# Kernel optimization log

Measured on AMD Instinct MI355X. Metric: run time of the kernel, lower is better.

Reference implementation:

```python
import jax, jax.numpy as jnp
import numpy as np

N_NODES = 51200      # 128 graphs * 400 ROIs
N_ROI = 400
HID = 64             # 'batch_size' arg of the torch module = hidden channels = n_timepoints
N_EDGES = 1638400    # avg degree 32
N_CLASSES = 2
NEG_SLOPE = 0.01


def setup_inputs():
    key = jax.random.key(0)
    ks = jax.random.split(key, 20)
    s = 0.05
    inp = {
        'x': jax.random.normal(ks[0], (N_NODES, HID), dtype=jnp.float32),
        'edge_index': jax.random.randint(ks[1], (2, N_EDGES), 0, N_NODES, dtype=jnp.int64),
        'edge_weight': jax.random.uniform(ks[2], (N_EDGES,), dtype=jnp.float32),
        # GCNConv weights stored [in, out]; biases [out]
        'W1': jax.random.normal(ks[3], (HID, HID), dtype=jnp.float32) * s,
        'b1': jnp.zeros((HID,), jnp.float32),
        'W2': jax.random.normal(ks[4], (HID, HID), dtype=jnp.float32) * s,
        'b2': jnp.zeros((HID,), jnp.float32),
        'W3': jax.random.normal(ks[5], (HID, HID), dtype=jnp.float32) * s,
        'b3': jnp.zeros((HID,), jnp.float32),
        'W4': jax.random.normal(ks[6], (HID, HID), dtype=jnp.float32) * s,
        'b4': jnp.zeros((HID,), jnp.float32),
        'fc1_w': jax.random.normal(ks[7], (N_ROI * HID, 256), dtype=jnp.float32) * 0.01,
        'fc1_b': jnp.zeros((256,), jnp.float32),
        'fc2_w': jax.random.normal(ks[8], (256, 128), dtype=jnp.float32) * s,
        'fc2_b': jnp.zeros((128,), jnp.float32),
        'fc3_w': jax.random.normal(ks[9], (128, N_CLASSES), dtype=jnp.float32) * s,
        'fc3_b': jnp.zeros((N_CLASSES,), jnp.float32),
    }
    return inp


def _gcn_norm(edge_index, edge_weight, n):
    # PyG GCNConv: add self-loops (weight 1), symmetric D^-1/2 A D^-1/2 normalization
    loop = jnp.arange(n, dtype=edge_index.dtype)
    src = jnp.concatenate([edge_index[0], loop])
    dst = jnp.concatenate([edge_index[1], loop])
    w = jnp.concatenate([edge_weight, jnp.ones((n,), edge_weight.dtype)])
    deg = jax.ops.segment_sum(w, dst, num_segments=n)
    dis = jnp.where(deg > 0, jax.lax.rsqrt(jnp.maximum(deg, 1e-30)), 0.0)
    norm = dis[src] * w * dis[dst]
    return src, dst, norm


def _conv(h, W, b, src, dst, norm, n):
    h = h @ W                                   # [N, out]
    msg = h[src] * norm[:, None]                # gather + scale
    out = jax.ops.segment_sum(msg, dst, num_segments=n) + b
    return out


def _leaky(v):
    return jnp.where(v >= 0, v, NEG_SLOPE * v)


def _head(h, fc1_w, fc1_b, fc2_w, fc2_b, fc3_w, fc3_b):
    # global_mean_pool with batch = arange(N) is identity; pool == reshape to graphs
    g = h.reshape(-1, N_ROI * HID)              # [G, n_roi*hid]
    g = g @ fc1_w + fc1_b                       # dropout is eval-mode identity
    g = g @ fc2_w + fc2_b
    g = g @ fc3_w + fc3_b
    return g


def reference(x, edge_index, edge_weight, W1, b1, W2, b2, W3, b3, W4, b4,
              fc1_w, fc1_b, fc2_w, fc2_b, fc3_w, fc3_b):
    n = x.shape[0]
    src, dst, norm = _gcn_norm(edge_index, edge_weight, n)
    h = _leaky(_conv(x, W1, b1, src, dst, norm, n))
    h = _leaky(_conv(h, W2, b2, src, dst, norm, n))
    h = _leaky(_conv(h, W3, b3, src, dst, norm, n))
    h = _leaky(_conv(h, W4, b4, src, dst, norm, n))
    logits = _head(h, fc1_w, fc1_b, fc2_w, fc2_b, fc3_w, fc3_b)
    logits0 = _head(x, fc1_w, fc1_b, fc2_w, fc2_b, fc3_w, fc3_b)
    penal = 0.09 * logits.shape[0] / jnp.linalg.norm(logits - logits0)
    return logits, penal
```

## Files before the change

### kernel.cpp

```cpp
#include <hip/hip_runtime.h>
#include <cstddef>

#define N_NODES 51200
#define N_EDGES 1638400
#define HID 64
#define N_ROI 400
#define N_GRAPHS 128
#define KHEAD 25600
#define NEG_SLOPE 0.01f
#define CAP 80
#define NCHUNK 400
#define CHUNK 4096
#define NBIN 800
#define BINSZ 64
#define LSTRIDE 81

typedef unsigned short u16;
typedef unsigned int u32;
typedef unsigned char u8;
typedef float f32x2 __attribute__((ext_vector_type(2)));

__device__ inline u16 f2bf(float f) {
    u32 u = __float_as_uint(f);
    u32 r = u + 0x7FFFu + ((u >> 16) & 1u);
    return (u16)(r >> 16);
}
__device__ inline float bf2f(u16 h) { return __uint_as_float(((u32)h) << 16); }

__device__ inline f32x2 dec8lo(u32 v) { return __builtin_amdgcn_cvt_pk_f32_fp8((int)v, false); }
__device__ inline f32x2 dec8hi(u32 v) { return __builtin_amdgcn_cvt_pk_f32_fp8((int)v, true); }
template <bool HI>
__device__ inline u32 enc8(float a, float b, u32 old) {
    return (u32)__builtin_amdgcn_cvt_pk_fp8_f32(a, b, (int)old, HI);
}
__device__ inline u32 pack4_fp8(float a, float b, float c, float d) {
    u32 w = enc8<false>(a, b, 0u);
    return enc8<true>(c, d, w);
}


__global__ __launch_bounds__(1024) void k1(const int* __restrict__ ei,
                                           const float* __restrict__ ew,
                                           uint2* __restrict__ chunkData,
                                           u32* __restrict__ offcnt,
                                           const float* __restrict__ x,
                                           u8* __restrict__ x8,
                                           const float* __restrict__ fc2w,
                                           const float* __restrict__ fc3w,
                                           const float* __restrict__ fc1b,
                                           const float* __restrict__ fc2b,
                                           const float* __restrict__ fc3b,
                                           float* __restrict__ fc23,
                                           float* __restrict__ bc) {
    int bid = blockIdx.x, t = threadIdx.x;
    __shared__ u32 cnt[1024];
    __shared__ u32 scan[1024];
    __shared__ u32 cur[1024];
    __shared__ uint2 stag[CHUNK];
    __shared__ float t1[128];

    if (bid < NCHUNK) {
        cnt[t] = 0;
        __syncthreads();
        int base = bid * CHUNK;
        u32 lo[4]; float wv[4]; int bin[4];
        #pragma unroll
        for (int i = 0; i < 4; i++) {
            int e = base + i * 1024 + t;
            int s = ei[e], d = ei[N_EDGES + e];
            wv[i] = ew[e];
            bin[i] = d >> 6;
            lo[i] = (u32)s | ((u32)(d & 63) << 16);
            atomicAdd(&cnt[bin[i]], 1u);
        }
        __syncthreads();
        scan[t] = cnt[t];
        __syncthreads();
        for (int off = 1; off < 1024; off <<= 1) {
            u32 add = (t >= off) ? scan[t - off] : 0u;
            __syncthreads();
            scan[t] += add;
            __syncthreads();
        }
        cur[t] = scan[t] - cnt[t];
        __syncthreads();
        if (t < NBIN) offcnt[bid * NBIN + t] = cur[t] | (cnt[t] << 16);
        __syncthreads();
        #pragma unroll
        for (int i = 0; i < 4; i++) {
            u32 pos = atomicAdd(&cur[bin[i]], 1u);
            stag[pos] = make_uint2(lo[i], __float_as_uint(wv[i]));
        }
        __syncthreads();
        #pragma unroll
        for (int i = 0; i < 4; i++)
            chunkData[base + i * 1024 + t] = stag[i * 1024 + t];
    } else if (bid < 600) {
        int idx = (bid - NCHUNK) * 1024 + t;
        const float4* xp = reinterpret_cast<const float4*>(x) + (size_t)idx * 4;
        float4 a = xp[0], b = xp[1], c = xp[2], d = xp[3];
        reinterpret_cast<uint4*>(x8)[idx] =
            make_uint4(pack4_fp8(a.x, a.y, a.z, a.w), pack4_fp8(b.x, b.y, b.z, b.w),
                       pack4_fp8(c.x, c.y, c.z, c.w), pack4_fp8(d.x, d.y, d.z, d.w));
    } else {
        if (t < 256) {
            float s0 = 0.f, s1 = 0.f;
            const float* row = fc2w + t * 128;
            for (int j = 0; j < 128; j++) {
                float a = row[j];
                s0 += a * fc3w[2 * j];
                s1 += a * fc3w[2 * j + 1];
            }
            fc23[2 * t] = s0;
            fc23[2 * t + 1] = s1;
        }
        if (t < 128) {
            float s = fc2b[t];
            for (int k = 0; k < 256; k++) s += fc1b[k] * fc2w[k * 128 + t];
            t1[t] = s;
        }
        __syncthreads();
        if (t < 2) {
            float s = fc3b[t];
            for (int j = 0; j < 128; j++) s += t1[j] * fc3w[2 * j + t];
            bc[t] = s;
        }
    }
}


__global__ __launch_bounds__(256) void k1t(const u32* __restrict__ in,
                                           u32* __restrict__ outT) {
    __shared__ u32 tile[32][33];
    int cx = blockIdx.x % 13, by = blockIdx.x / 13;
    int c0 = cx * 32, b0 = by * 32;
    int tx = threadIdx.x & 31, ty = threadIdx.x >> 5;
    for (int i = ty; i < 32; i += 8) {
        int c = c0 + i;
        if (c < NCHUNK) tile[i][tx] = in[(size_t)c * NBIN + b0 + tx];
    }
    __syncthreads();
    for (int i = ty; i < 32; i += 8) {
        int b = b0 + i;
        int c = c0 + tx;
        if (c < NCHUNK) outT[(size_t)b * NCHUNK + c] = tile[tx][i];
    }
}


__global__ __launch_bounds__(512) void k2(const uint2* __restrict__ chunkData,
                                          const u32* __restrict__ offcntT,
                                          u32* __restrict__ buck,
                                          int* __restrict__ cnts,
                                          float* __restrict__ dis,
                                          const float* __restrict__ fc1w,
                                          const float* __restrict__ fc23,
                                          float* __restrict__ Wc) {
    int bid = blockIdx.x, t = threadIdx.x;
    __shared__ u32 lbuck[BINSZ * LSTRIDE];
    __shared__ u32 lcnt[BINSZ];
    __shared__ float ldeg[BINSZ];
    __shared__ u32 oc[NCHUNK];
    __shared__ float f23[512];

    if (bid < NBIN) {
        if (t < BINSZ) { lcnt[t] = 0; ldeg[t] = 0.f; }
        if (t < NCHUNK) oc[t] = offcntT[(size_t)bid * NCHUNK + t];
        __syncthreads();
        if (t < NCHUNK) {
            u32 o = oc[t];
            int off = (int)(o & 0xffffu), k = (int)(o >> 16);
            const uint2* cd = chunkData + (size_t)t * CHUNK + off;
            for (int i = 0; i < k; i++) {
                uint2 e = cd[i];
                u32 node = e.x >> 16;
                u32 src = e.x & 0xffffu;
                float w = __uint_as_float(e.y);
                u32 pos = atomicAdd(&lcnt[node], 1u);
                if (pos < CAP - 1) lbuck[node * LSTRIDE + pos] = ((u32)f2bf(w) << 16) | src;
                atomicAdd(&ldeg[node], w);
            }
        }
        __syncthreads();
        int sg = t >> 5, ln = t & 31;
        for (int n = sg; n < BINSZ; n += 16) {
            int node = bid * BINSZ + n;
            int k = min((int)lcnt[n], CAP - 1);
            u32* dst = buck + (size_t)node * CAP;
            for (int i = ln; i < k; i += 32) dst[i] = lbuck[n * LSTRIDE + i];
            if (ln == 0) {
                cnts[node] = k;
                dis[node] = rsqrtf(1.f + ldeg[n]);
            }
        }
    } else {
        f23[t] = fc23[t];
        __syncthreads();
        int r = (bid - NBIN) * 512 + t;
        const float* row = fc1w + (size_t)r * 256;
        float s0 = 0.f, s1 = 0.f;
        #pragma unroll 8
        for (int k = 0; k < 256; k++) {
            float a = row[k];
            s0 += a * f23[2 * k];
            s1 += a * f23[2 * k + 1];
        }
        Wc[2 * r] = s0;
        Wc[2 * r + 1] = s1;
    }
}


__global__ __launch_bounds__(1024) void k3(u32* __restrict__ buck,
                                           int* __restrict__ cnts,
                                           const float* __restrict__ dis) {
    int gt = blockIdx.x * 1024 + threadIdx.x;
    int node = gt >> 5, sub = gt & 31;
    float d = dis[node];
    int k = cnts[node];
    u32* bk = buck + (size_t)node * CAP;
    for (int j = sub; j < k; j += 32) {
        u32 e = bk[j];
        float val = bf2f((u16)(e >> 16)) * d * dis[e & 0xffffu];
        bk[j] = ((u32)f2bf(val) << 16) | (e & 0xffffu);
    }
    if (sub == 0) {
        bk[k] = ((u32)f2bf(d * d) << 16) | (u32)node;
        cnts[node] = k + 1;
    }
}


__global__ __launch_bounds__(512) void k_layer(const u8* __restrict__ H8,
                                               const u32* __restrict__ buck,
                                               const int* __restrict__ cnts,
                                               const float* __restrict__ W,
                                               const float* __restrict__ bias,
                                               u8* __restrict__ Hout) {
    __shared__ float Ws[64][64];
    __shared__ float ZsT[64][33];
    int t = threadIdx.x;
    int base = blockIdx.x * 32;

    #pragma unroll
    for (int i = 0; i < 2; i++) {
        int f = t + i * 512;
        int kk = f >> 4, c4 = f & 15;
        float4 wv = reinterpret_cast<const float4*>(W)[f];
        *reinterpret_cast<float4*>(&Ws[kk][c4 * 4]) = wv;
    }

    int grp = t >> 4, sub = t & 15;
    int node = base + grp;
    int k = cnts[node];
    const u32* bk = buck + (size_t)node * CAP;
    const u8* Hb = H8 + sub * 4;
    float a0 = 0.f, a1 = 0.f, a2 = 0.f, a3 = 0.f;
    for (int j0 = 0; j0 < k; j0 += 16) {
        int idx = j0 + sub;
        u32 pre = (idx < k) ? bk[idx] : 0u;
        #pragma unroll
        for (int i = 0; i < 16; i++) {
            u32 e = (u32)__shfl((int)pre, i, 16);
            float val = __uint_as_float(e & 0xffff0000u);
            u32 src = e & 0xffffu;
            u32 r = *reinterpret_cast<const u32*>(Hb + (size_t)src * HID);
            f32x2 lo = dec8lo(r), hi = dec8hi(r);
            a0 += val * lo.x; a1 += val * lo.y;
            a2 += val * hi.x; a3 += val * hi.y;
        }
    }
    ZsT[4 * sub + 0][grp] = a0;
    ZsT[4 * sub + 1][grp] = a1;
    ZsT[4 * sub + 2][grp] = a2;
    ZsT[4 * sub + 3][grp] = a3;
    __syncthreads();

    int r = t >> 4, c4 = t & 15;
    float4 acc = {0.f, 0.f, 0.f, 0.f};
    #pragma unroll 8
    for (int kk = 0; kk < 64; kk++) {
        float a = ZsT[kk][r];
        const float4 w = *reinterpret_cast<const float4*>(&Ws[kk][c4 * 4]);
        acc.x += a * w.x; acc.y += a * w.y; acc.z += a * w.z; acc.w += a * w.w;
    }
    float4 bb = reinterpret_cast<const float4*>(bias)[c4];
    float v0 = acc.x + bb.x, v1 = acc.y + bb.y, v2 = acc.z + bb.z, v3 = acc.w + bb.w;
    v0 = v0 >= 0.f ? v0 : NEG_SLOPE * v0;
    v1 = v1 >= 0.f ? v1 : NEG_SLOPE * v1;
    v2 = v2 >= 0.f ? v2 : NEG_SLOPE * v2;
    v3 = v3 >= 0.f ? v3 : NEG_SLOPE * v3;
    *reinterpret_cast<u32*>(Hout + (size_t)(base + r) * HID + c4 * 4) =
        pack4_fp8(v0, v1, v2, v3);
}


__global__ __launch_bounds__(256) void k_logits(const u8* __restrict__ h4,
                                                const float* __restrict__ x,
                                                const float* __restrict__ Wc,
                                                const float* __restrict__ bc,
                                                float* __restrict__ out,
                                                float* __restrict__ sq,
                                                int* __restrict__ done) {
    int g = blockIdx.x, t = threadIdx.x;
    const u8* bh = h4 + (size_t)g * KHEAD;
    const float* bx = x + (size_t)g * KHEAD;
    float aH0 = 0.f, aH1 = 0.f, aX0 = 0.f, aX1 = 0.f;
    for (int k2 = t; k2 < KHEAD / 2; k2 += 256) {
        u32 hv = reinterpret_cast<const u16*>(bh)[k2];
        f32x2 h = dec8lo(hv);
        float2 xv = reinterpret_cast<const float2*>(bx)[k2];
        float4 wc = reinterpret_cast<const float4*>(Wc)[k2];
        aH0 += h.x * wc.x + h.y * wc.z;
        aH1 += h.x * wc.y + h.y * wc.w;
        aX0 += xv.x * wc.x + xv.y * wc.z;
        aX1 += xv.x * wc.y + xv.y * wc.w;
    }
    for (int off = 32; off > 0; off >>= 1) {
        aH0 += __shfl_down(aH0, off);
        aH1 += __shfl_down(aH1, off);
        aX0 += __shfl_down(aX0, off);
        aX1 += __shfl_down(aX1, off);
    }
    __shared__ float red[4][4];
    int wave = t >> 6, lane = t & 63;
    if (lane == 0) {
        red[wave][0] = aH0; red[wave][1] = aH1;
        red[wave][2] = aX0; red[wave][3] = aX1;
    }
    __syncthreads();
    if (t == 0) {
        float h0 = red[0][0] + red[1][0] + red[2][0] + red[3][0];
        float h1 = red[0][1] + red[1][1] + red[2][1] + red[3][1];
        float x0 = red[0][2] + red[1][2] + red[2][2] + red[3][2];
        float x1 = red[0][3] + red[1][3] + red[2][3] + red[3][3];
        out[2 * g]     = h0 + bc[0];
        out[2 * g + 1] = h1 + bc[1];
        float d0 = h0 - x0, d1 = h1 - x1;
        atomicAdd(sq, d0 * d0 + d1 * d1);
        __threadfence();
        int c = atomicAdd(done, 1);
        if (c == N_GRAPHS - 1) {
            __threadfence();
            float s = atomicAdd(sq, 0.f);
            out[2 * N_GRAPHS] = 0.09f * (float)N_GRAPHS / sqrtf(s);
        }
    }
}


extern "C" void kernel_launch(void* const* d_in, const int* in_sizes, int n_in,
                              void* d_out, int out_size, void* d_ws, size_t ws_size,
                              hipStream_t stream) {
    const float* x    = (const float*)d_in[0];
    const int*   ei   = (const int*)d_in[1];
    const float* ew   = (const float*)d_in[2];
    const float* W1   = (const float*)d_in[3];
    const float* b1   = (const float*)d_in[4];
    const float* W2   = (const float*)d_in[5];
    const float* b2   = (const float*)d_in[6];
    const float* W3   = (const float*)d_in[7];
    const float* b3   = (const float*)d_in[8];
    const float* W4   = (const float*)d_in[9];
    const float* b4   = (const float*)d_in[10];
    const float* fc1w = (const float*)d_in[11];
    const float* fc1b = (const float*)d_in[12];
    const float* fc2w = (const float*)d_in[13];
    const float* fc2b = (const float*)d_in[14];
    const float* fc3w = (const float*)d_in[15];
    const float* fc3b = (const float*)d_in[16];
    float* out = (float*)d_out;

    char* base = (char*)d_ws;
    size_t off = 0;
    auto alloc = [&](size_t bytes) -> void* {
        void* p = base + off;
        off += (bytes + 255) & ~(size_t)255;
        return p;
    };
    uint2* chunkData = (uint2*)alloc((size_t)N_EDGES * 8);
    u32*   offcnt    = (u32*)alloc((size_t)NCHUNK * NBIN * 4);
    u32*   offcntT   = (u32*)alloc((size_t)NCHUNK * NBIN * 4);
    u32*   buck      = (u32*)alloc((size_t)N_NODES * CAP * 4);
    int*   cnts      = (int*)alloc((size_t)N_NODES * 4);
    float* dis       = (float*)alloc((size_t)N_NODES * 4);
    u8*    x8        = (u8*)alloc((size_t)N_NODES * HID);
    u8*    ha        = (u8*)alloc((size_t)N_NODES * HID);
    u8*    hb        = (u8*)alloc((size_t)N_NODES * HID);
    float* fc23      = (float*)alloc(512 * 4);
    float* bc        = (float*)alloc(2 * 4);
    float* Wc        = (float*)alloc((size_t)KHEAD * 2 * 4);
    char*  ctrl      = (char*)alloc(256);
    float* sq        = (float*)ctrl;
    int*   done      = (int*)(ctrl + 4);

    (void)hipMemsetAsync(ctrl, 0, 8, stream);
    k1<<<601, 1024, 0, stream>>>(ei, ew, chunkData, offcnt, x, x8,
                                 fc2w, fc3w, fc1b, fc2b, fc3b, fc23, bc);
    k1t<<<13 * 25, 256, 0, stream>>>(offcnt, offcntT);
    k2<<<NBIN + 50, 512, 0, stream>>>(chunkData, offcntT, buck, cnts, dis,
                                      fc1w, fc23, Wc);
    k3<<<1600, 1024, 0, stream>>>(buck, cnts, dis);

    const float* Wl[4] = {W1, W2, W3, W4};
    const float* bl[4] = {b1, b2, b3, b4};
    u8* hbufs[2] = {ha, hb};
    const u8* hin = x8;
    for (int l = 0; l < 4; l++) {
        u8* hout = hbufs[l & 1];
        k_layer<<<N_NODES / 32, 512, 0, stream>>>(hin, buck, cnts,
                                                  Wl[l], bl[l], hout);
        hin = hout;
    }

    k_logits<<<N_GRAPHS, 256, 0, stream>>>(hin, x, Wc, bc, out, sq, done);
}
```

Before: 199.7 us.

## Use 512 bins of 100 nodes and spread per-chunk edge reads across lanes

Destination nodes are now bucketed into 512 bins of 100 nodes instead of 800 bins of 64. The bin index is computed with integer division, and the scan runs only over the active bins. In the bucketing kernel, each wavefront now covers 50 chunks, with 8 lanes striding over each chunk's edges, instead of one thread walking a whole chunk serially. This spreads the serial per-chunk loop across lanes and coalesces the reads. The trade-off is fewer blocks and more atomic contention per bin. The fc23 shared buffer is aliased onto lbuck to save LDS.

```diff
diff --git a/kernel.cpp b/kernel.cpp
--- a/kernel.cpp
+++ b/kernel.cpp
@@ -11,8 +11,8 @@
 #define CAP 80
 #define NCHUNK 400
 #define CHUNK 4096
-#define NBIN 800
-#define BINSZ 64
+#define NBIN 512
+#define BINSZ 100
 #define LSTRIDE 81
 
 typedef unsigned short u16;
@@ -53,14 +53,14 @@
                                            float* __restrict__ fc23,
                                            float* __restrict__ bc) {
     int bid = blockIdx.x, t = threadIdx.x;
-    __shared__ u32 cnt[1024];
-    __shared__ u32 scan[1024];
-    __shared__ u32 cur[1024];
+    __shared__ u32 cnt[NBIN];
+    __shared__ u32 scan[NBIN];
+    __shared__ u32 cur[NBIN];
     __shared__ uint2 stag[CHUNK];
     __shared__ float t1[128];
 
     if (bid < NCHUNK) {
-        cnt[t] = 0;
+        if (t < NBIN) cnt[t] = 0;
         __syncthreads();
         int base = bid * CHUNK;
         u32 lo[4]; float wv[4]; int bin[4];
@@ -69,22 +69,22 @@
             int e = base + i * 1024 + t;
             int s = ei[e], d = ei[N_EDGES + e];
             wv[i] = ew[e];
-            bin[i] = d >> 6;
-            lo[i] = (u32)s | ((u32)(d & 63) << 16);
+            bin[i] = d / BINSZ;
+            lo[i] = (u32)s | ((u32)(d - bin[i] * BINSZ) << 16);
             atomicAdd(&cnt[bin[i]], 1u);
         }
         __syncthreads();
-        scan[t] = cnt[t];
-        __syncthreads();
-        for (int off = 1; off < 1024; off <<= 1) {
-            u32 add = (t >= off) ? scan[t - off] : 0u;
+        if (t < NBIN) scan[t] = cnt[t];
+        __syncthreads();
+        for (int off = 1; off < NBIN; off <<= 1) {
+            u32 add = (t < NBIN && t >= off) ? scan[t - off] : 0u;
             __syncthreads();
-            scan[t] += add;
+            if (t < NBIN) scan[t] += add;
             __syncthreads();
         }
-        cur[t] = scan[t] - cnt[t];
-        __syncthreads();
-        if (t < NBIN) offcnt[bid * NBIN + t] = cur[t] | (cnt[t] << 16);
+        if (t < NBIN) cur[t] = scan[t] - cnt[t];
+        __syncthreads();
+        if (t < NBIN) offcnt[(size_t)bid * NBIN + t] = cur[t] | (cnt[t] << 16);
         __syncthreads();
         #pragma unroll
         for (int i = 0; i < 4; i++) {
@@ -161,24 +161,31 @@
     __shared__ u32 lcnt[BINSZ];
     __shared__ float ldeg[BINSZ];
     __shared__ u32 oc[NCHUNK];
-    __shared__ float f23[512];
 
     if (bid < NBIN) {
         if (t < BINSZ) { lcnt[t] = 0; ldeg[t] = 0.f; }
         if (t < NCHUNK) oc[t] = offcntT[(size_t)bid * NCHUNK + t];
         __syncthreads();
-        if (t < NCHUNK) {
-            u32 o = oc[t];
-            int off = (int)(o & 0xffffu), k = (int)(o >> 16);
-            const uint2* cd = chunkData + (size_t)t * CHUNK + off;
-            for (int i = 0; i < k; i++) {
+        int w = t >> 6, lane = t & 63;
+        int sBase = w * 50;
+        for (int j = 0; j < 56; j += 8) {
+            int s = sBase + j + (lane >> 3);
+            int i0 = lane & 7;
+            int k = 0, off = 0;
+            if (j + (lane >> 3) < 50) {
+                u32 o = oc[s];
+                off = (int)(o & 0xffffu);
+                k = (int)(o >> 16);
+            }
+            const uint2* cd = chunkData + (size_t)s * CHUNK + off;
+            for (int i = i0; i < k; i += 8) {
                 uint2 e = cd[i];
                 u32 node = e.x >> 16;
                 u32 src = e.x & 0xffffu;
-                float w = __uint_as_float(e.y);
+                float ww = __uint_as_float(e.y);
                 u32 pos = atomicAdd(&lcnt[node], 1u);
-                if (pos < CAP - 1) lbuck[node * LSTRIDE + pos] = ((u32)f2bf(w) << 16) | src;
-                atomicAdd(&ldeg[node], w);
+                if (pos < CAP - 1) lbuck[node * LSTRIDE + pos] = ((u32)f2bf(ww) << 16) | src;
+                atomicAdd(&ldeg[node], ww);
             }
         }
         __syncthreads();
@@ -194,6 +201,7 @@
             }
         }
     } else {
+        float* f23 = (float*)lbuck;
         f23[t] = fc23[t];
         __syncthreads();
         int r = (bid - NBIN) * 512 + t;
@@ -397,7 +405,7 @@
     (void)hipMemsetAsync(ctrl, 0, 8, stream);
     k1<<<601, 1024, 0, stream>>>(ei, ew, chunkData, offcnt, x, x8,
                                  fc2w, fc3w, fc1b, fc2b, fc3b, fc23, bc);
-    k1t<<<13 * 25, 256, 0, stream>>>(offcnt, offcntT);
+    k1t<<<13 * 16, 256, 0, stream>>>(offcnt, offcntT);
     k2<<<NBIN + 50, 512, 0, stream>>>(chunkData, offcntT, buck, cnts, dis,
                                       fc1w, fc23, Wc);
     k3<<<1600, 1024, 0, stream>>>(buck, cnts, dis);
```

After: 192.1 us. 3.8% less time.
